# Kernel optimization log

Measured on AMD Instinct MI355X. Metric: run time of the kernel, lower is better.

## Reference

```python
import jax, jax.numpy as jnp
import numpy as np

DIM = 64        # feature size per vector
CODES = 512     # codebook size (called d_model in the torch module)
DECAY = 0.99
EPS = 1e-5


def setup_inputs() -> dict:
    key = jax.random.key(0)
    k1, k2 = jax.random.split(key)
    x = jax.random.normal(k1, (64, 64, 64, 64), dtype=jnp.float32)
    embedding = jax.random.normal(k2, (DIM, CODES), dtype=jnp.float32)
    N = jnp.zeros((CODES,), dtype=jnp.float32)
    M = embedding.copy()  # torch module initializes M as embedding.clone()
    return {"x": x, "embedding": embedding, "N": N, "M": M}


def reference(x, embedding, N, M):
    # flatten tokens: [T, DIM]
    flatten = x.reshape(-1, DIM)
    # squared L2 distance to every code: [T, CODES]
    distance = (jnp.sum(flatten * flatten, axis=1, keepdims=True)
                - 2.0 * flatten @ embedding
                + jnp.sum(embedding * embedding, axis=0, keepdims=True))
    max_index = jnp.argmin(distance, axis=1)          # (-distance).max(1) == argmin
    indices = max_index.reshape(x.shape[:-1])
    # gather codes: embedding.T is [CODES, DIM]
    quantize = jnp.take(embedding.T, max_index, axis=0).reshape(x.shape)

    # EMA codebook update (training=True). Avoid materializing onehot:
    # ni = onehot.sum(0); eofx = flatten.T @ onehot  -> segment sums over codes.
    ni = jax.ops.segment_sum(jnp.ones_like(max_index, dtype=jnp.float32),
                             max_index, num_segments=CODES)          # [CODES]
    eofx = jax.ops.segment_sum(flatten, max_index, num_segments=CODES).T  # [DIM, CODES]
    N_new = N * DECAY + (1.0 - DECAY) * ni
    M_new = M * DECAY + (1.0 - DECAY) * eofx
    n = jnp.sum(N_new)
    N_smoothed = (N_new + EPS) / (n + CODES * EPS) * n
    embedding_new = M_new / N_smoothed

    quant_loss = jnp.mean((jax.lax.stop_gradient(x) - quantize) ** 2)
    commitment_loss = jnp.mean((jax.lax.stop_gradient(quantize) - x) ** 2)
    quantize_st = x + jax.lax.stop_gradient(quantize - x)  # straight-through
    return (quantize_st, quant_loss, indices, commitment_loss,
            embedding_new, N_new, M_new)
```

## Files before the change

kernel.cpp:

```cpp
#include <hip/hip_runtime.h>
#include <hip/hip_bf16.h>
#include <math.h>

#define DIM 64
#define CODES 512
#define TOKENS 262144
#define XELEMS 16777216

#define DECAYF 0.99f
#define OMDECAY 0.01f
#define EPSF 1e-5f

#define WS_CNORM 0
#define WS_NI    512
#define WS_EOFX  1024
#define WS_LOSS  33792
#define WS_ET    33808
#define WS_IMG   66576
#define WS_IDX   99344
#define WS_PART  361488
#define PART_STRIDE 33280

#define OFF_Q    0
#define OFF_QL   16777216
#define OFF_IDX  16777217
#define OFF_CL   17039361
#define OFF_ENEW 17039362
#define OFF_NNEW 17072130
#define OFF_MNEW 17072642

typedef __attribute__((ext_vector_type(8))) short bf16x8;
typedef __attribute__((ext_vector_type(4))) float f32x4;

static __device__ inline void split_bf(float v, short& hi, short& lo) {
  unsigned int b = __float_as_uint(v);
  unsigned int hb = b & 0xffff0000u;
  float lof = v - __uint_as_float(hb);
  hi = (short)(b >> 16);
  lo = (short)(__float_as_uint(lof) >> 16);
}

__global__ __launch_bounds__(256) void vq_prep(const float* __restrict__ emb,
                                               float* __restrict__ ws) {
  int c = blockIdx.x * 256 + threadIdx.x;
  unsigned short* img = (unsigned short*)(ws + WS_IMG);
  float* eT = ws + WS_ET;
  int cc = c >> 4;
  int n = c & 15;
  float cn = 0.f;
#pragma unroll
  for (int d0 = 0; d0 < DIM; d0 += 4) {
    float v[4];
#pragma unroll
    for (int u = 0; u < 4; ++u) {
      v[u] = emb[(d0 + u) * CODES + c];
      cn = fmaf(v[u], v[u], cn);
    }
    *(float4*)(eT + (size_t)c * DIM + d0) = make_float4(v[0], v[1], v[2], v[3]);
    int kh = d0 >> 5, kk = d0 & 31, qd = kk >> 3, j0 = kk & 7;
    int lane = qd * 16 + n;
    short hi[4], lo[4];
#pragma unroll
    for (int u = 0; u < 4; ++u) split_bf(v[u], hi[u], lo[u]);
    int base = cc * 2048 + kh * 1024 + lane * 8 + j0;
    *(ushort4*)(img + base) =
        make_ushort4((unsigned short)hi[0], (unsigned short)hi[1],
                     (unsigned short)hi[2], (unsigned short)hi[3]);
    *(ushort4*)(img + base + 512) =
        make_ushort4((unsigned short)lo[0], (unsigned short)lo[1],
                     (unsigned short)lo[2], (unsigned short)lo[3]);
  }
  ws[WS_CNORM + c] = cn;
}

__global__ __launch_bounds__(512, 2) void vq_fused(
    const float* __restrict__ x, const float* __restrict__ ws,
    float* __restrict__ loss_sum, float* __restrict__ q_out,
    float* __restrict__ idx_out, int* __restrict__ idx_int) {
  __shared__ __align__(16) unsigned short bimg[65536];
  __shared__ float cn_l[CODES];

  const float* eT = ws + WS_ET;

  {
    const float4* src = (const float4*)(ws + WS_IMG);
    float4* dst = (float4*)bimg;
    for (int i = threadIdx.x; i < 8192; i += 512) dst[i] = src[i];
    for (int i = threadIdx.x; i < CODES; i += 512) cn_l[i] = ws[WS_CNORM + i];
  }
  __syncthreads();

  const int lane = threadIdx.x & 63;
  const int wave = threadIdx.x >> 6;
  const int n = lane & 15;
  const int quad = lane >> 4;
  const int t0 = blockIdx.x * 512 + wave * 64;

  bf16x8 ah[4][2], al[4][2];
#pragma unroll
  for (int tile = 0; tile < 4; ++tile) {
    const float* xr = x + (size_t)(t0 + tile * 16 + n) * DIM + quad * 8;
#pragma unroll
    for (int kh = 0; kh < 2; ++kh) {
      float4 v0 = *(const float4*)(xr + kh * 32);
      float4 v1 = *(const float4*)(xr + kh * 32 + 4);
      float f[8] = {v0.x, v0.y, v0.z, v0.w, v1.x, v1.y, v1.z, v1.w};
#pragma unroll
      for (int j = 0; j < 8; ++j) {
        short hi, lo;
        split_bf(-2.f * f[j], hi, lo);
        ah[tile][kh][j] = hi;
        al[tile][kh][j] = lo;
      }
    }
  }

  float v1[4][4], v2[4][4];
  int i1[4][4], i2[4][4];
#pragma unroll
  for (int tile = 0; tile < 4; ++tile)
#pragma unroll
    for (int r = 0; r < 4; ++r) {
      v1[tile][r] = 1e30f;
      v2[tile][r] = 1e30f;
      i1[tile][r] = 0x3FFFFFFF;
      i2[tile][r] = 0x3FFFFFFF;
    }

  for (int cc = 0; cc < 32; ++cc) {
    const unsigned short* bp = bimg + cc * 2048;
    bf16x8 bh0 = *(const bf16x8*)(bp + lane * 8);
    bf16x8 bl0 = *(const bf16x8*)(bp + 512 + lane * 8);
    bf16x8 bh1 = *(const bf16x8*)(bp + 1024 + lane * 8);
    bf16x8 bl1 = *(const bf16x8*)(bp + 1536 + lane * 8);
    float cnv = cn_l[cc * 16 + n];
    int cid = cc * 16 + n;
#pragma unroll
    for (int tile = 0; tile < 4; ++tile) {
      f32x4 acc = {0.f, 0.f, 0.f, 0.f};
      acc = __builtin_amdgcn_mfma_f32_16x16x32_bf16(ah[tile][0], bh0, acc, 0, 0, 0);
      acc = __builtin_amdgcn_mfma_f32_16x16x32_bf16(al[tile][0], bh0, acc, 0, 0, 0);
      acc = __builtin_amdgcn_mfma_f32_16x16x32_bf16(ah[tile][0], bl0, acc, 0, 0, 0);
      acc = __builtin_amdgcn_mfma_f32_16x16x32_bf16(ah[tile][1], bh1, acc, 0, 0, 0);
      acc = __builtin_amdgcn_mfma_f32_16x16x32_bf16(al[tile][1], bh1, acc, 0, 0, 0);
      acc = __builtin_amdgcn_mfma_f32_16x16x32_bf16(ah[tile][1], bl1, acc, 0, 0, 0);
#pragma unroll
      for (int r = 0; r < 4; ++r) {
        float s = acc[r] + cnv;
        bool c1 = s < v1[tile][r];
        bool c2 = s < v2[tile][r];
        i2[tile][r] = c1 ? i1[tile][r] : (c2 ? cid : i2[tile][r]);
        v2[tile][r] = fminf(fmaxf(s, v1[tile][r]), v2[tile][r]);
        i1[tile][r] = c1 ? cid : i1[tile][r];
        v1[tile][r] = fminf(s, v1[tile][r]);
      }
    }
  }

#pragma unroll
  for (int m = 1; m < 16; m <<= 1) {
#pragma unroll
    for (int tile = 0; tile < 4; ++tile)
#pragma unroll
      for (int r = 0; r < 4; ++r) {
        float ov1 = __shfl_xor(v1[tile][r], m, 16);
        int oi1 = __shfl_xor(i1[tile][r], m, 16);
        float ov2 = __shfl_xor(v2[tile][r], m, 16);
        int oi2 = __shfl_xor(i2[tile][r], m, 16);
        bool f = ov1 < v1[tile][r];
        float hi = f ? v1[tile][r] : ov1;
        int hii = f ? i1[tile][r] : oi1;
        v1[tile][r] = f ? ov1 : v1[tile][r];
        i1[tile][r] = f ? oi1 : i1[tile][r];
        bool g = ov2 < v2[tile][r];
        float lo2 = g ? ov2 : v2[tile][r];
        int lo2i = g ? oi2 : i2[tile][r];
        bool e2 = hi < lo2;
        v2[tile][r] = e2 ? hi : lo2;
        i2[tile][r] = e2 ? hii : lo2i;
      }
  }

  float loss = 0.f;
#pragma unroll
  for (int tile = 0; tile < 4; ++tile) {
#pragma unroll
    for (int r = 0; r < 4; ++r) {
      int t = t0 + tile * 16 + quad * 4 + r;
      int c1 = i1[tile][r];
      int c2 = i2[tile][r];
      float4 xv = *(const float4*)(x + (size_t)t * DIM + n * 4);
      float4 e1 = *(const float4*)(eT + (size_t)c1 * DIM + n * 4);
      float4 e2 = *(const float4*)(eT + (size_t)c2 * DIM + n * 4);
      float p1 = xv.x * e1.x;
      p1 = fmaf(xv.y, e1.y, p1);
      p1 = fmaf(xv.z, e1.z, p1);
      p1 = fmaf(xv.w, e1.w, p1);
      float p2 = xv.x * e2.x;
      p2 = fmaf(xv.y, e2.y, p2);
      p2 = fmaf(xv.z, e2.z, p2);
      p2 = fmaf(xv.w, e2.w, p2);
#pragma unroll
      for (int m = 1; m < 16; m <<= 1) {
        p1 += __shfl_xor(p1, m, 16);
        p2 += __shfl_xor(p2, m, 16);
      }
      float d1 = fmaf(-2.f, p1, cn_l[c1]);
      float d2 = fmaf(-2.f, p2, cn_l[c2]);
      bool take2 = (d2 < d1) || (d2 == d1 && c2 < c1);
      int w = take2 ? c2 : c1;
      float4 q = take2 ? e2 : e1;
      *(float4*)(q_out + (size_t)t * DIM + n * 4) = q;
      float u0 = xv.x - q.x, u1 = xv.y - q.y;
      float u2 = xv.z - q.z, u3 = xv.w - q.w;
      loss = fmaf(u0, u0, loss);
      loss = fmaf(u1, u1, loss);
      loss = fmaf(u2, u2, loss);
      loss = fmaf(u3, u3, loss);
      if (n == 0) {
        idx_out[t] = (float)w;
        idx_int[t] = w;
      }
    }
  }
#pragma unroll
  for (int off = 32; off > 0; off >>= 1) loss += __shfl_down(loss, off, 64);
  if (lane == 0) atomicAdd(loss_sum, loss);
}

__global__ __launch_bounds__(256, 1) void vq_segsum(
    const float* __restrict__ x, const int* __restrict__ idx,
    float* __restrict__ dest_base, int tokens_per_block, int part_stride,
    int aflush) {
  __shared__ float lds_n[CODES];
  __shared__ float lds_e[DIM * CODES];
  int p = blockIdx.x;
  int t0 = p * tokens_per_block;
  float* dest = dest_base + (size_t)p * part_stride;

  {
    float4 z = make_float4(0.f, 0.f, 0.f, 0.f);
    float4* zn = (float4*)lds_n;
    float4* ze = (float4*)lds_e;
    for (int i = threadIdx.x; i < CODES / 4; i += 256) zn[i] = z;
    for (int i = threadIdx.x; i < DIM * CODES / 4; i += 256) ze[i] = z;
  }
  __syncthreads();

  for (int tt = threadIdx.x; tt < tokens_per_block; tt += 256) {
    int t = t0 + tt;
    int bi = idx[t];
    atomicAdd(&lds_n[bi], 1.0f);
    const float4* xp = (const float4*)(x + (size_t)t * DIM);
#pragma unroll
    for (int i = 0; i < DIM / 4; ++i) {
      float4 v = xp[i];
      atomicAdd(&lds_e[(4 * i + 0) * CODES + bi], v.x);
      atomicAdd(&lds_e[(4 * i + 1) * CODES + bi], v.y);
      atomicAdd(&lds_e[(4 * i + 2) * CODES + bi], v.z);
      atomicAdd(&lds_e[(4 * i + 3) * CODES + bi], v.w);
    }
  }
  __syncthreads();

  for (int i = threadIdx.x; i < DIM * CODES; i += 256) {
    float v = lds_e[i];
    if (aflush) {
      if (v != 0.f) atomicAdd(&dest[CODES + i], v);
    } else {
      dest[CODES + i] = v;
    }
  }
  for (int i = threadIdx.x; i < CODES; i += 256) {
    float v = lds_n[i];
    if (aflush) {
      if (v != 0.f) atomicAdd(&dest[i], v);
    } else {
      dest[i] = v;
    }
  }
}

__global__ __launch_bounds__(256) void vq_reduce(const float* __restrict__ part,
                                                 float* __restrict__ ws, int P) {
  int i = blockIdx.x * 256 + threadIdx.x;
  if (i >= PART_STRIDE) return;
  float a0 = 0.f, a1 = 0.f, a2 = 0.f, a3 = 0.f;
  int p = 0;
  for (; p + 3 < P; p += 4) {
    a0 += part[(size_t)(p + 0) * PART_STRIDE + i];
    a1 += part[(size_t)(p + 1) * PART_STRIDE + i];
    a2 += part[(size_t)(p + 2) * PART_STRIDE + i];
    a3 += part[(size_t)(p + 3) * PART_STRIDE + i];
  }
  for (; p < P; ++p) a0 += part[(size_t)p * PART_STRIDE + i];
  ws[WS_NI + i] = (a0 + a1) + (a2 + a3);
}

__global__ __launch_bounds__(512) void vq_final(const float* __restrict__ Nin,
                                                const float* __restrict__ Min,
                                                const float* __restrict__ ws,
                                                float* __restrict__ out) {
  __shared__ float red[512];
  int c = threadIdx.x;
  int d = blockIdx.x;
  float niv = ws[WS_NI + c];
  float Nn = Nin[c] * DECAYF + OMDECAY * niv;
  red[c] = Nn;
  __syncthreads();
#pragma unroll
  for (int s = 256; s > 0; s >>= 1) {
    if (c < s) red[c] += red[c + s];
    __syncthreads();
  }
  float nsum = red[0];
  float Nsm = (Nn + EPSF) / (nsum + (float)CODES * EPSF) * nsum;
  float m = Min[d * CODES + c] * DECAYF + OMDECAY * ws[WS_EOFX + d * CODES + c];
  out[OFF_MNEW + d * CODES + c] = m;
  out[OFF_ENEW + d * CODES + c] = m / Nsm;
  if (d == 0) {
    out[OFF_NNEW + c] = Nn;
    if (c == 0) {
      float l = ws[WS_LOSS] / (float)XELEMS;
      out[OFF_QL] = l;
      out[OFF_CL] = l;
    }
  }
}

extern "C" void kernel_launch(void* const* d_in, const int* in_sizes, int n_in,
                              void* d_out, int out_size, void* d_ws, size_t ws_size,
                              hipStream_t stream) {
  const float* x = (const float*)d_in[0];
  const float* emb = (const float*)d_in[1];
  const float* Nin = (const float*)d_in[2];
  const float* Min = (const float*)d_in[3];
  float* out = (float*)d_out;
  float* ws = (float*)d_ws;
  int* idxw = (int*)(ws + WS_IDX);

  size_t avail = ws_size / 4;
  int P = 0;
  if (avail > (size_t)WS_PART) {
    size_t cap = (avail - WS_PART) / PART_STRIDE;
    P = 256;
    while (P > (int)cap) P >>= 1;
    if (P < 64) P = 0;
  }

  hipMemsetAsync(ws + WS_NI, 0, (size_t)(WS_ET - WS_NI) * sizeof(float), stream);

  vq_prep<<<2, 256, 0, stream>>>(emb, ws);

  vq_fused<<<TOKENS / 512, 512, 0, stream>>>(
      x, ws, ws + WS_LOSS, out + OFF_Q, out + OFF_IDX, idxw);

  if (P > 0) {
    vq_segsum<<<P, 256, 0, stream>>>(x, idxw, ws + WS_PART, TOKENS / P,
                                     PART_STRIDE, 0);
    vq_reduce<<<(PART_STRIDE + 255) / 256, 256, 0, stream>>>(ws + WS_PART, ws, P);
  } else {
    vq_segsum<<<256, 256, 0, stream>>>(x, idxw, ws + WS_NI, TOKENS / 256, 0, 1);
  }

  vq_final<<<DIM, 512, 0, stream>>>(Nin, Min, ws, out);
}
```

Measured before the change: 388.4 us.

## Fuse segment-sum into distance kernel and pack code index into float mantissa

The separate segment-sum kernel goes away. Each fused block reuses its shared memory to accumulate per-code counts and feature sums for its 512 tokens, using x values rebuilt from the bf16 hi/lo registers. It then writes per-block partials, reduced over 512 partials, or flushes atomically to the workspace. The top-2 tracking now packs the code index into the low 9 mantissa bits of the distance, so a single min/med3 replaces the separate index compare-selects. This removes a second pass over x and the index buffer round trip. In exchange it adds LDS atomics, a larger partial reduction, and a small loss of distance precision in the low bits, which the exact rescoring of the top two candidates compensates for.

Result: faster. 361.2 us (-7.0%).

```diff
diff --git a/kernel.cpp b/kernel.cpp
--- a/kernel.cpp
+++ b/kernel.cpp
@@ -17,9 +17,9 @@
 #define WS_LOSS  33792
 #define WS_ET    33808
 #define WS_IMG   66576
-#define WS_IDX   99344
-#define WS_PART  361488
+#define WS_PART  99344
 #define PART_STRIDE 33280
+#define NPART 512
 
 #define OFF_Q    0
 #define OFF_QL   16777216
@@ -38,6 +38,10 @@
   float lof = v - __uint_as_float(hb);
   hi = (short)(b >> 16);
   lo = (short)(__float_as_uint(lof) >> 16);
+}
+static __device__ inline float bf2f(short s) {
+  unsigned int u = ((unsigned int)(unsigned short)s) << 16;
+  return __uint_as_float(u);
 }
 
 __global__ __launch_bounds__(256) void vq_prep(const float* __restrict__ emb,
@@ -76,9 +80,14 @@
 __global__ __launch_bounds__(512, 2) void vq_fused(
     const float* __restrict__ x, const float* __restrict__ ws,
     float* __restrict__ loss_sum, float* __restrict__ q_out,
-    float* __restrict__ idx_out, int* __restrict__ idx_int) {
-  __shared__ __align__(16) unsigned short bimg[65536];
-  __shared__ float cn_l[CODES];
+    float* __restrict__ idx_out, float* __restrict__ part_base, int aflush,
+    float* __restrict__ ws_acc) {
+  __shared__ __align__(16) unsigned char smem[135424];
+  unsigned short* bimg = (unsigned short*)smem;
+  float* cn_l = (float*)(smem + 131072);
+  int* win_l = (int*)(smem + 133376);
+  float* lds_n = (float*)smem;
+  float* lds_e = (float*)(smem + 2048);
 
   const float* eT = ws + WS_ET;
 
@@ -103,8 +112,8 @@
 #pragma unroll
     for (int kh = 0; kh < 2; ++kh) {
       float4 v0 = *(const float4*)(xr + kh * 32);
-      float4 v1 = *(const float4*)(xr + kh * 32 + 4);
-      float f[8] = {v0.x, v0.y, v0.z, v0.w, v1.x, v1.y, v1.z, v1.w};
+      float4 v1v = *(const float4*)(xr + kh * 32 + 4);
+      float f[8] = {v0.x, v0.y, v0.z, v0.w, v1v.x, v1v.y, v1v.z, v1v.w};
 #pragma unroll
       for (int j = 0; j < 8; ++j) {
         short hi, lo;
@@ -115,16 +124,14 @@
     }
   }
 
+  const float INITP = __uint_as_float((__float_as_uint(1e30f) & 0xFFFFFE00u) | 511u);
   float v1[4][4], v2[4][4];
-  int i1[4][4], i2[4][4];
 #pragma unroll
   for (int tile = 0; tile < 4; ++tile)
 #pragma unroll
     for (int r = 0; r < 4; ++r) {
-      v1[tile][r] = 1e30f;
-      v2[tile][r] = 1e30f;
-      i1[tile][r] = 0x3FFFFFFF;
-      i2[tile][r] = 0x3FFFFFFF;
+      v1[tile][r] = INITP;
+      v2[tile][r] = INITP;
     }
 
   for (int cc = 0; cc < 32; ++cc) {
@@ -134,7 +141,7 @@
     bf16x8 bh1 = *(const bf16x8*)(bp + 1024 + lane * 8);
     bf16x8 bl1 = *(const bf16x8*)(bp + 1536 + lane * 8);
     float cnv = cn_l[cc * 16 + n];
-    int cid = cc * 16 + n;
+    unsigned int cid = (unsigned int)(cc * 16 + n);
 #pragma unroll
     for (int tile = 0; tile < 4; ++tile) {
       f32x4 acc = {0.f, 0.f, 0.f, 0.f};
@@ -147,12 +154,10 @@
 #pragma unroll
       for (int r = 0; r < 4; ++r) {
         float s = acc[r] + cnv;
-        bool c1 = s < v1[tile][r];
-        bool c2 = s < v2[tile][r];
-        i2[tile][r] = c1 ? i1[tile][r] : (c2 ? cid : i2[tile][r]);
-        v2[tile][r] = fminf(fmaxf(s, v1[tile][r]), v2[tile][r]);
-        i1[tile][r] = c1 ? cid : i1[tile][r];
-        v1[tile][r] = fminf(s, v1[tile][r]);
+        float sp = __uint_as_float((__float_as_uint(s) & 0xFFFFFE00u) | cid);
+        float o1 = v1[tile][r];
+        v2[tile][r] = __builtin_amdgcn_fmed3f(sp, o1, v2[tile][r]);
+        v1[tile][r] = fminf(sp, o1);
       }
     }
   }
@@ -163,21 +168,11 @@
     for (int tile = 0; tile < 4; ++tile)
 #pragma unroll
       for (int r = 0; r < 4; ++r) {
-        float ov1 = __shfl_xor(v1[tile][r], m, 16);
-        int oi1 = __shfl_xor(i1[tile][r], m, 16);
-        float ov2 = __shfl_xor(v2[tile][r], m, 16);
-        int oi2 = __shfl_xor(i2[tile][r], m, 16);
-        bool f = ov1 < v1[tile][r];
-        float hi = f ? v1[tile][r] : ov1;
-        int hii = f ? i1[tile][r] : oi1;
-        v1[tile][r] = f ? ov1 : v1[tile][r];
-        i1[tile][r] = f ? oi1 : i1[tile][r];
-        bool g = ov2 < v2[tile][r];
-        float lo2 = g ? ov2 : v2[tile][r];
-        int lo2i = g ? oi2 : i2[tile][r];
-        bool e2 = hi < lo2;
-        v2[tile][r] = e2 ? hi : lo2;
-        i2[tile][r] = e2 ? hii : lo2i;
+        float o1 = __shfl_xor(v1[tile][r], m, 16);
+        float o2 = __shfl_xor(v2[tile][r], m, 16);
+        float a = v1[tile][r];
+        v1[tile][r] = fminf(a, o1);
+        v2[tile][r] = fminf(fminf(v2[tile][r], o2), fmaxf(a, o1));
       }
   }
 
@@ -187,8 +182,8 @@
 #pragma unroll
     for (int r = 0; r < 4; ++r) {
       int t = t0 + tile * 16 + quad * 4 + r;
-      int c1 = i1[tile][r];
-      int c2 = i2[tile][r];
+      int c1 = (int)(__float_as_uint(v1[tile][r]) & 511u);
+      int c2 = (int)(__float_as_uint(v2[tile][r]) & 511u);
       float4 xv = *(const float4*)(x + (size_t)t * DIM + n * 4);
       float4 e1 = *(const float4*)(eT + (size_t)c1 * DIM + n * 4);
       float4 e2 = *(const float4*)(eT + (size_t)c2 * DIM + n * 4);
@@ -219,64 +214,54 @@
       loss = fmaf(u3, u3, loss);
       if (n == 0) {
         idx_out[t] = (float)w;
-        idx_int[t] = w;
+        win_l[wave * 64 + tile * 16 + quad * 4 + r] = w;
       }
     }
   }
 #pragma unroll
   for (int off = 32; off > 0; off >>= 1) loss += __shfl_down(loss, off, 64);
   if (lane == 0) atomicAdd(loss_sum, loss);
-}
-
-__global__ __launch_bounds__(256, 1) void vq_segsum(
-    const float* __restrict__ x, const int* __restrict__ idx,
-    float* __restrict__ dest_base, int tokens_per_block, int part_stride,
-    int aflush) {
-  __shared__ float lds_n[CODES];
-  __shared__ float lds_e[DIM * CODES];
-  int p = blockIdx.x;
-  int t0 = p * tokens_per_block;
-  float* dest = dest_base + (size_t)p * part_stride;
-
+
+  __syncthreads();
   {
     float4 z = make_float4(0.f, 0.f, 0.f, 0.f);
-    float4* zn = (float4*)lds_n;
-    float4* ze = (float4*)lds_e;
-    for (int i = threadIdx.x; i < CODES / 4; i += 256) zn[i] = z;
-    for (int i = threadIdx.x; i < DIM * CODES / 4; i += 256) ze[i] = z;
-  }
-  __syncthreads();
-
-  for (int tt = threadIdx.x; tt < tokens_per_block; tt += 256) {
-    int t = t0 + tt;
-    int bi = idx[t];
-    atomicAdd(&lds_n[bi], 1.0f);
-    const float4* xp = (const float4*)(x + (size_t)t * DIM);
-#pragma unroll
-    for (int i = 0; i < DIM / 4; ++i) {
-      float4 v = xp[i];
-      atomicAdd(&lds_e[(4 * i + 0) * CODES + bi], v.x);
-      atomicAdd(&lds_e[(4 * i + 1) * CODES + bi], v.y);
-      atomicAdd(&lds_e[(4 * i + 2) * CODES + bi], v.z);
-      atomicAdd(&lds_e[(4 * i + 3) * CODES + bi], v.w);
-    }
-  }
-  __syncthreads();
-
-  for (int i = threadIdx.x; i < DIM * CODES; i += 256) {
-    float v = lds_e[i];
-    if (aflush) {
-      if (v != 0.f) atomicAdd(&dest[CODES + i], v);
-    } else {
-      dest[CODES + i] = v;
-    }
-  }
-  for (int i = threadIdx.x; i < CODES; i += 256) {
-    float v = lds_n[i];
-    if (aflush) {
-      if (v != 0.f) atomicAdd(&dest[i], v);
-    } else {
-      dest[i] = v;
+    float4* zp = (float4*)smem;
+    for (int i = threadIdx.x; i < 133376 / 16; i += 512) zp[i] = z;
+  }
+  __syncthreads();
+
+#pragma unroll
+  for (int tile = 0; tile < 4; ++tile) {
+    int wbi = win_l[wave * 64 + tile * 16 + n];
+    if (quad == 0) atomicAdd(&lds_n[wbi], 1.0f);
+#pragma unroll
+    for (int kh = 0; kh < 2; ++kh) {
+#pragma unroll
+      for (int j = 0; j < 8; ++j) {
+        float xk = -0.5f * (bf2f(ah[tile][kh][j]) + bf2f(al[tile][kh][j]));
+        int k = kh * 32 + quad * 8 + j;
+        atomicAdd(&lds_e[k * 513 + wbi], xk);
+      }
+    }
+  }
+  __syncthreads();
+
+  if (aflush) {
+    for (int i = threadIdx.x; i < CODES; i += 512) {
+      float v = lds_n[i];
+      if (v != 0.f) atomicAdd(&ws_acc[WS_NI + i], v);
+    }
+    for (int i = threadIdx.x; i < DIM * CODES; i += 512) {
+      int k = i >> 9, c = i & 511;
+      float v = lds_e[k * 513 + c];
+      if (v != 0.f) atomicAdd(&ws_acc[WS_EOFX + i], v);
+    }
+  } else {
+    float* dest = part_base + (size_t)blockIdx.x * PART_STRIDE;
+    for (int i = threadIdx.x; i < CODES; i += 512) dest[i] = lds_n[i];
+    for (int i = threadIdx.x; i < DIM * CODES; i += 512) {
+      int k = i >> 9, c = i & 511;
+      dest[CODES + i] = lds_e[k * 513 + c];
     }
   }
 }
@@ -337,30 +322,20 @@
   const float* Min = (const float*)d_in[3];
   float* out = (float*)d_out;
   float* ws = (float*)d_ws;
-  int* idxw = (int*)(ws + WS_IDX);
 
   size_t avail = ws_size / 4;
-  int P = 0;
-  if (avail > (size_t)WS_PART) {
-    size_t cap = (avail - WS_PART) / PART_STRIDE;
-    P = 256;
-    while (P > (int)cap) P >>= 1;
-    if (P < 64) P = 0;
-  }
+  int aflush = (avail < (size_t)WS_PART + (size_t)NPART * PART_STRIDE) ? 1 : 0;
 
   hipMemsetAsync(ws + WS_NI, 0, (size_t)(WS_ET - WS_NI) * sizeof(float), stream);
 
   vq_prep<<<2, 256, 0, stream>>>(emb, ws);
 
   vq_fused<<<TOKENS / 512, 512, 0, stream>>>(
-      x, ws, ws + WS_LOSS, out + OFF_Q, out + OFF_IDX, idxw);
-
-  if (P > 0) {
-    vq_segsum<<<P, 256, 0, stream>>>(x, idxw, ws + WS_PART, TOKENS / P,
-                                     PART_STRIDE, 0);
-    vq_reduce<<<(PART_STRIDE + 255) / 256, 256, 0, stream>>>(ws + WS_PART, ws, P);
-  } else {
-    vq_segsum<<<256, 256, 0, stream>>>(x, idxw, ws + WS_NI, TOKENS / 256, 0, 1);
+      x, ws, ws + WS_LOSS, out + OFF_Q, out + OFF_IDX, ws + WS_PART, aflush, ws);
+
+  if (!aflush) {
+    vq_reduce<<<(PART_STRIDE + 255) / 256, 256, 0, stream>>>(ws + WS_PART, ws,
+                                                             NPART);
   }
 
   vq_final<<<DIM, 512, 0, stream>>>(Nin, Min, ws, out);
```
